# Kernel optimization log

Measured on AMD Instinct MI355X. Metric: run time of the kernel, lower is better.

Reference implementation:

```python
import jax, jax.numpy as jnp
import numpy as np
from jax import lax

# config (matches init_kwargs)
HEADS = 4
KD2 = 256          # key_dim // 2
KNN = 16
BLOCK = 128        # knn * block_rate
COL = 512          # value_size // block
VALUE_SIZE = 65536 # key_num ** 2
D_OUT = 512
D_IN = 1024
QUERYDIM = HEADS * KD2  # 1024
KERNEL = 3


def setup_inputs() -> dict:
    key = jax.random.key(0)
    ks = jax.random.split(key, 8)
    B, T = 2, 2048
    return {
        "x": jax.random.normal(ks[0], (B, T, D_IN), dtype=jnp.float32),
        "conv_w": jax.random.normal(ks[1], (D_IN, 1, KERNEL), dtype=jnp.float32) * 0.1,
        "conv_b": jax.random.normal(ks[2], (D_IN,), dtype=jnp.float32) * 0.1,
        "lin_w": jax.random.normal(ks[3], (QUERYDIM, D_IN), dtype=jnp.float32) * (D_IN ** -0.5),
        "lin_b": jax.random.normal(ks[4], (QUERYDIM,), dtype=jnp.float32) * 0.1,
        "rowkeys": jax.random.normal(ks[5], (BLOCK, HEADS, KD2), dtype=jnp.float32) * (KD2 ** -0.5),
        "colkeys": jax.random.normal(ks[6], (COL, HEADS, KD2), dtype=jnp.float32) * (KD2 ** -0.5),
        "value_w": jax.random.normal(ks[7], (VALUE_SIZE, D_OUT), dtype=jnp.float32),
    }


def _forward(x, conv_w, conv_b, lin_w, lin_b, rowkeys, colkeys, value_w):
    B, T, C = x.shape
    # --- Querynet: causal depthwise conv1d + linear ---
    xt = jnp.transpose(x, (0, 2, 1))  # (B, C, T)
    y = lax.conv_general_dilated(
        xt, conv_w, window_strides=(1,), padding=[(KERNEL - 1, 0)],
        feature_group_count=C, dimension_numbers=("NCH", "OIH", "NCH"))
    y = y + conv_b[None, :, None]
    y = jnp.transpose(y, (0, 2, 1))                     # (B, T, C)
    query = y @ lin_w.T + lin_b                         # (B, T, querydim)
    # torch: query.view(B, heads, T, key_dim//2) -- raw C-order reshape
    q = query.reshape(B, HEADS, T, KD2)
    # --- block_wise_choice.get_indices ---
    score = jnp.einsum("bhtd,ehd->bhte", q, rowkeys)    # (B,H,T,block)
    col_scores = jnp.einsum("bhtd,chd->bhtc", q, colkeys)  # (B,H,T,col)
    score_col, idx_col = lax.top_k(col_scores, 1)       # (B,H,T,1)
    base = jnp.arange(BLOCK, dtype=jnp.int32)
    indices = base[None, None, None, :] * COL + idx_col  # (B,H,T,block)
    score = score + score_col                            # broadcast add
    # torch .view(B,H,-1,T): raw C-order reshape mixing tokens and blocks
    score = score.reshape(B, HEADS, BLOCK, T)
    indices = indices.reshape(B, HEADS, BLOCK, T)
    k = T * KNN // BLOCK
    score_top, dispatch = lax.top_k(score, k)            # (B,H,block,k), sorted desc
    idx_top = jnp.take_along_axis(indices, dispatch, axis=-1)
    score_r = score_top.reshape(B, BLOCK, -1)            # (B, block, H*k)
    idx_r = idx_top.reshape(B, BLOCK, -1)
    disp_r = dispatch.reshape(B, BLOCK, -1)
    # --- Memory_value: gather-weight-scatter ---
    gathered = value_w[idx_r]                            # (B, block, H*k, d)
    weighted = (gathered * score_r[..., None]).reshape(B, -1, D_OUT)
    flat_disp = disp_r.reshape(B, -1)                    # values in [0, T)
    out = jnp.zeros((B, T, D_OUT), dtype=weighted.dtype)
    out = out.at[jnp.arange(B)[:, None], flat_disp].add(weighted)
    return out


def reference(x, conv_w, conv_b, lin_w, lin_b, rowkeys, colkeys, value_w):
    return _forward(x, conv_w, conv_b, lin_w, lin_b, rowkeys, colkeys, value_w)
```

## Files before the change

kernel.cpp:

```cpp
#include <hip/hip_runtime.h>

constexpr int Bc   = 2;
constexpr int Tc   = 2048;
constexpr int Cc   = 1024;
constexpr int QDc  = 1024;
constexpr int Hc   = 4;
constexpr int KD2c = 256;
constexpr int BLKc = 128;
constexpr int COLc = 512;
constexpr int DOUTc= 512;
constexpr int KSELc= 256;
constexpr int NKEYS= BLKc + COLc;
constexpr int NBINS= Bc * Tc;
constexpr int NSEL = Bc * Hc * BLKc * KSELc;

typedef short bf16x8 __attribute__((ext_vector_type(8)));
typedef float f32x4  __attribute__((ext_vector_type(4)));

__device__ __forceinline__ unsigned short f2bf(float f) {
    unsigned u = __float_as_uint(f);
    u += 0x7FFFu + ((u >> 16) & 1u);
    return (unsigned short)(u >> 16);
}
__device__ __forceinline__ float bf2f(unsigned short h) {
    return __uint_as_float((unsigned)h << 16);
}
__device__ __forceinline__ void splitbf3(float f, unsigned short* h,
                                         unsigned short* m, unsigned short* l) {
    unsigned short hh = f2bf(f);
    float r1 = f - bf2f(hh);
    unsigned short mm = f2bf(r1);
    float r2 = r1 - bf2f(mm);
    *h = hh; *m = mm; *l = f2bf(r2);
}

__device__ __forceinline__ void gld_lds16(const void* g, void* l) {
    __builtin_amdgcn_global_load_lds(
        (const __attribute__((address_space(1))) unsigned int*)g,
        (__attribute__((address_space(3))) unsigned int*)l, 16, 0, 0);
}

__global__ __launch_bounds__(256) void conv_kernel(
    const float* __restrict__ x, const float* __restrict__ cw,
    const float* __restrict__ cb, unsigned short* __restrict__ y1,
    unsigned short* __restrict__ y2, unsigned short* __restrict__ y3)
{
    int idx = blockIdx.x * 256 + threadIdx.x;
    int c = idx & (Cc - 1);
    int t = (idx >> 10) & (Tc - 1);
    int b = idx >> 21;
    float w0 = cw[c*3+0], w1 = cw[c*3+1], w2 = cw[c*3+2];
    const float* xb = x + (size_t)b * Tc * Cc;
    float acc = cb[c] + w2 * xb[(size_t)t*Cc + c];
    if (t >= 1) acc += w1 * xb[(size_t)(t-1)*Cc + c];
    if (t >= 2) acc += w0 * xb[(size_t)(t-2)*Cc + c];
    splitbf3(acc, &y1[idx], &y2[idx], &y3[idx]);
}

__global__ __launch_bounds__(256) void convw_kernel(
    const float* __restrict__ w, unsigned short* __restrict__ w1,
    unsigned short* __restrict__ w2, unsigned short* __restrict__ w3)
{
    int idx = blockIdx.x * 256 + threadIdx.x;
    splitbf3(w[idx], &w1[idx], &w2[idx], &w3[idx]);
}

__global__ __launch_bounds__(256) void convkeys_kernel(
    const float* __restrict__ rowkeys, const float* __restrict__ colkeys,
    unsigned short* __restrict__ k1, unsigned short* __restrict__ k2,
    unsigned short* __restrict__ k3)
{
    int bid = blockIdx.x;
    int h = bid / NKEYS, n = bid % NKEYS;
    int k = threadIdx.x;
    float v = (n < BLKc) ? rowkeys[((size_t)n*Hc + h)*KD2c + k]
                         : colkeys[((size_t)(n-BLKc)*Hc + h)*KD2c + k];
    size_t o = ((size_t)h*NKEYS + n)*KD2c + k;
    splitbf3(v, &k1[o], &k2[o], &k3[o]);
}

__device__ __forceinline__ void mfma_gemm_tile(
    const unsigned short* __restrict__ A1g, const unsigned short* __restrict__ A2g,
    const unsigned short* __restrict__ A3g, int lda,
    const unsigned short* __restrict__ B1g, const unsigned short* __restrict__ B2g,
    const unsigned short* __restrict__ B3g, int ldb,
    int K, int m0, int n0, char* lds, f32x4 acc[4][4])
{
    const int tid  = threadIdx.x;
    const int wave = tid >> 6, lane = tid & 63;
    const int wr = wave >> 1, wc = wave & 1;
    const int g = lane >> 4, r16 = lane & 15;

    int aoff[4], boff[4];
    #pragma unroll
    for (int i = 0; i < 4; i++) {
        int ra = wr*64 + i*16 + r16;
        aoff[i] = ra*64 + ((g ^ ((ra>>1)&3)) << 4);
        int rb = wc*64 + i*16 + r16;
        boff[i] = rb*64 + ((g ^ ((rb>>1)&3)) << 4);
    }
    const int c0 = wave*64 + lane;
    const int c1 = 256 + c0;
    const int row0 = c0 >> 2, kg0 = ((c0 & 3) ^ ((row0>>1)&3)) * 8;
    const int row1 = c1 >> 2, kg1 = ((c1 & 3) ^ ((row1>>1)&3)) * 8;
    char* d0 = lds + wave*1024;
    char* d1 = lds + 4096 + wave*1024;

#define STAGE(kc, bo) do {                                                 \
        size_t a0_ = (size_t)(m0+row0)*lda + (kc) + kg0;                   \
        size_t a1_ = (size_t)(m0+row1)*lda + (kc) + kg1;                   \
        size_t b0_ = (size_t)(n0+row0)*ldb + (kc) + kg0;                   \
        size_t b1_ = (size_t)(n0+row1)*ldb + (kc) + kg1;                   \
        gld_lds16(A1g + a0_, d0 + (bo));                                   \
        gld_lds16(A1g + a1_, d1 + (bo));                                   \
        gld_lds16(A2g + a0_, d0 + 8192 + (bo));                            \
        gld_lds16(A2g + a1_, d1 + 8192 + (bo));                            \
        gld_lds16(A3g + a0_, d0 + 16384 + (bo));                           \
        gld_lds16(A3g + a1_, d1 + 16384 + (bo));                           \
        gld_lds16(B1g + b0_, d0 + 24576 + (bo));                           \
        gld_lds16(B1g + b1_, d1 + 24576 + (bo));                           \
        gld_lds16(B2g + b0_, d0 + 32768 + (bo));                           \
        gld_lds16(B2g + b1_, d1 + 32768 + (bo));                           \
        gld_lds16(B3g + b0_, d0 + 40960 + (bo));                           \
        gld_lds16(B3g + b1_, d1 + 40960 + (bo));                           \
    } while (0)

    auto compute = [&](int bo) {
        bf16x8 a1[4], a2[4], a3[4], b1[4], b2[4], b3[4];
        #pragma unroll
        for (int i = 0; i < 4; i++) {
            a1[i] = *(const bf16x8*)(lds + bo + aoff[i]);
            a2[i] = *(const bf16x8*)(lds + bo +  8192 + aoff[i]);
            a3[i] = *(const bf16x8*)(lds + bo + 16384 + aoff[i]);
            b1[i] = *(const bf16x8*)(lds + bo + 24576 + boff[i]);
            b2[i] = *(const bf16x8*)(lds + bo + 32768 + boff[i]);
            b3[i] = *(const bf16x8*)(lds + bo + 40960 + boff[i]);
        }
        #pragma unroll
        for (int i = 0; i < 4; i++)
            #pragma unroll
            for (int j = 0; j < 4; j++) {
                acc[i][j] = __builtin_amdgcn_mfma_f32_16x16x32_bf16(a3[i], b1[j], acc[i][j], 0, 0, 0);
                acc[i][j] = __builtin_amdgcn_mfma_f32_16x16x32_bf16(a2[i], b2[j], acc[i][j], 0, 0, 0);
                acc[i][j] = __builtin_amdgcn_mfma_f32_16x16x32_bf16(a1[i], b3[j], acc[i][j], 0, 0, 0);
                acc[i][j] = __builtin_amdgcn_mfma_f32_16x16x32_bf16(a2[i], b1[j], acc[i][j], 0, 0, 0);
                acc[i][j] = __builtin_amdgcn_mfma_f32_16x16x32_bf16(a1[i], b2[j], acc[i][j], 0, 0, 0);
                acc[i][j] = __builtin_amdgcn_mfma_f32_16x16x32_bf16(a1[i], b1[j], acc[i][j], 0, 0, 0);
            }
    };

    const int NT = K / 32;
    STAGE(0, 0);
    int bo = 0;
    for (int t = 0; t < NT - 1; ++t) {
        STAGE((t+1)*32, bo ^ 49152);
        asm volatile("s_waitcnt vmcnt(12)" ::: "memory");
        __builtin_amdgcn_s_barrier();
        asm volatile("" ::: "memory");
        compute(bo);
        asm volatile("" ::: "memory");
        __builtin_amdgcn_s_barrier();
        bo ^= 49152;
    }
    asm volatile("s_waitcnt vmcnt(0)" ::: "memory");
    __builtin_amdgcn_s_barrier();
    asm volatile("" ::: "memory");
    compute(bo);
#undef STAGE
}

__global__ __launch_bounds__(256) void qgemm_kernel(
    const unsigned short* __restrict__ y1, const unsigned short* __restrict__ y2,
    const unsigned short* __restrict__ y3,
    const unsigned short* __restrict__ w1, const unsigned short* __restrict__ w2,
    const unsigned short* __restrict__ w3,
    const float* __restrict__ bias,
    unsigned short* __restrict__ q1, unsigned short* __restrict__ q2,
    unsigned short* __restrict__ q3)
{
    __shared__ char lds[98304];
    int m0 = blockIdx.y * 128, n0 = blockIdx.x * 128;
    f32x4 acc[4][4];
    #pragma unroll
    for (int i = 0; i < 4; i++)
        #pragma unroll
        for (int j = 0; j < 4; j++) acc[i][j] = (f32x4)0.f;
    mfma_gemm_tile(y1, y2, y3, Cc, w1, w2, w3, Cc, Cc, m0, n0, lds, acc);

    const int lane = threadIdx.x & 63, wave = threadIdx.x >> 6;
    const int wr = wave >> 1, wc = wave & 1;
    const int g = lane >> 4, r16 = lane & 15;
    #pragma unroll
    for (int i = 0; i < 4; i++)
        #pragma unroll
        for (int j = 0; j < 4; j++)
            #pragma unroll
            for (int reg = 0; reg < 4; reg++) {
                int m = m0 + wr*64 + i*16 + g*4 + reg;
                int n = n0 + wc*64 + j*16 + r16;
                float v = acc[i][j][reg] + bias[n];
                size_t o = (size_t)m * QDc + n;
                splitbf3(v, &q1[o], &q2[o], &q3[o]);
            }
}

__global__ __launch_bounds__(256) void sgemm_kernel(
    const unsigned short* __restrict__ q1, const unsigned short* __restrict__ q2,
    const unsigned short* __restrict__ q3,
    const unsigned short* __restrict__ k1, const unsigned short* __restrict__ k2,
    const unsigned short* __restrict__ k3,
    float* __restrict__ Ctmp)
{
    __shared__ char lds[98304];
    int b4h = blockIdx.z;
    size_t qo = (size_t)b4h * (Tc * KD2c);
    size_t ko = (size_t)(b4h & 3) * (NKEYS * KD2c);
    int m0 = blockIdx.y * 128, n0 = blockIdx.x * 128;
    f32x4 acc[4][4];
    #pragma unroll
    for (int i = 0; i < 4; i++)
        #pragma unroll
        for (int j = 0; j < 4; j++) acc[i][j] = (f32x4)0.f;
    mfma_gemm_tile(q1+qo, q2+qo, q3+qo, KD2c, k1+ko, k2+ko, k3+ko, KD2c,
                   KD2c, m0, n0, lds, acc);

    const int lane = threadIdx.x & 63, wave = threadIdx.x >> 6;
    const int wr = wave >> 1, wc = wave & 1;
    const int g = lane >> 4, r16 = lane & 15;
    float* Cb = Ctmp + (size_t)b4h * Tc * NKEYS;
    #pragma unroll
    for (int i = 0; i < 4; i++)
        #pragma unroll
        for (int j = 0; j < 4; j++)
            #pragma unroll
            for (int reg = 0; reg < 4; reg++) {
                int m = m0 + wr*64 + i*16 + g*4 + reg;
                int n = n0 + wc*64 + j*16 + r16;
                Cb[(size_t)m * NKEYS + n] = acc[i][j][reg];
            }
}

__global__ __launch_bounds__(256) void colmax_kernel(
    const float* __restrict__ Ctmp, float* __restrict__ s, int* __restrict__ cidx)
{
    int rid = blockIdx.x * 4 + (threadIdx.x >> 6);
    int lane = threadIdx.x & 63;
    const float* row = Ctmp + (size_t)rid * NKEYS;
    float best = -3.4e38f; int bi = 0;
    #pragma unroll
    for (int i = 0; i < 8; i++) {
        int c = lane + i*64;
        float v = row[BLKc + c];
        if (v > best) { best = v; bi = c; }
    }
    #pragma unroll
    for (int off = 32; off > 0; off >>= 1) {
        float ov = __shfl_xor(best, off, 64);
        int   oi = __shfl_xor(bi,   off, 64);
        if (ov > best || (ov == best && oi < bi)) { best = ov; bi = oi; }
    }
    if (lane == 0) cidx[rid] = bi;
    #pragma unroll
    for (int e = lane; e < BLKc; e += 64)
        s[(size_t)rid*BLKc + e] = row[e] + best;
}

__global__ __launch_bounds__(256) void topk_kernel(
    const float* __restrict__ s, const int* __restrict__ cidx,
    int* __restrict__ tk_j, int* __restrict__ tk_vidx, float* __restrict__ tk_score)
{
    int wid  = (blockIdx.x << 2) + (threadIdx.x >> 6);
    int lane = threadIdx.x & 63;
    int batch = wid >> 7;
    int i = wid & 127;
    const float* srow = s + (size_t)batch * (Tc*BLKc) + (size_t)i * 2048;

    unsigned key[8][4];
    #pragma unroll
    for (int r = 0; r < 8; r++) {
        float4 v4 = *(const float4*)&srow[r*256 + lane*4];
        float vv[4] = {v4.x, v4.y, v4.z, v4.w};
        #pragma unroll
        for (int e = 0; e < 4; e++) {
            unsigned u = __float_as_uint(vv[e]);
            key[r][e] = (u >> 31) ? ~u : (u | 0x80000000u);
        }
    }

    unsigned lo = 0, hi = 0xFFFFFFFFu;
    while (lo < hi) {
        unsigned d = hi - lo;
        unsigned mid = lo + ((d >> 1) + (d & 1u));
        int cnt = 0;
        #pragma unroll
        for (int r = 0; r < 8; r++)
            #pragma unroll
            for (int e = 0; e < 4; e++)
                cnt += (key[r][e] >= mid) ? 1 : 0;
        #pragma unroll
        for (int off = 32; off > 0; off >>= 1) cnt += __shfl_xor(cnt, off, 64);
        if (cnt >= KSELc) lo = mid; else hi = mid - 1;
    }
    const unsigned thr = lo;

    int gcnt = 0, ecnt = 0;
    unsigned eqmask = 0;
    #pragma unroll
    for (int r = 0; r < 8; r++)
        #pragma unroll
        for (int e = 0; e < 4; e++) {
            gcnt += (key[r][e] > thr) ? 1 : 0;
            if (key[r][e] == thr) { eqmask |= (1u << (r*4+e)); ecnt++; }
        }

    int gpre = gcnt, epre = ecnt;
    #pragma unroll
    for (int off = 1; off < 64; off <<= 1) {
        int gv = __shfl_up(gpre, off, 64);
        int ev = __shfl_up(epre, off, 64);
        if (lane >= off) { gpre += gv; epre += ev; }
    }
    const int total_greater = __shfl(gpre, 63, 64);
    const int total_eq      = __shfl(epre, 63, 64);
    const int gbase = gpre - gcnt;
    const int ebase = epre - ecnt;
    const int need  = KSELc - total_greater;

    const size_t obase = (size_t)wid * KSELc;
    const int cbase = batch * Tc + i * 16;

    int rk = 0;
    #pragma unroll
    for (int r = 0; r < 8; r++)
        #pragma unroll
        for (int e = 0; e < 4; e++) {
            if (key[r][e] > thr) {
                int j = r*256 + lane*4 + e;
                unsigned u = key[r][e];
                float f = (u >> 31) ? __uint_as_float(u ^ 0x80000000u)
                                    : __uint_as_float(~u);
                size_t o = obase + gbase + rk;
                tk_j[o] = j;
                tk_vidx[o] = (j & 127) * COLc + cidx[cbase + (j >> 7)];
                tk_score[o] = f;
                rk++;
            }
        }

    if (need == total_eq) {
        int erk = 0;
        #pragma unroll
        for (int r = 0; r < 8; r++)
            #pragma unroll
            for (int e = 0; e < 4; e++) {
                if (key[r][e] == thr) {
                    int j = r*256 + lane*4 + e;
                    float f = (thr >> 31) ? __uint_as_float(thr ^ 0x80000000u)
                                          : __uint_as_float(~thr);
                    size_t o = obase + total_greater + ebase + erk;
                    tk_j[o] = j;
                    tk_vidx[o] = (j & 127) * COLc + cidx[cbase + (j >> 7)];
                    tk_score[o] = f;
                    erk++;
                }
            }
    } else {
        unsigned em = eqmask;
        int left = need;
        while (left > 0) {
            int myj = 0x7FFFFFFF;
            if (em) {
                int bit = __builtin_ctz(em);
                myj = (bit >> 2)*256 + lane*4 + (bit & 3);
            }
            int mn = myj;
            #pragma unroll
            for (int off = 32; off > 0; off >>= 1) mn = min(mn, __shfl_xor(mn, off, 64));
            if (myj == mn) {
                em &= em - 1;
                int j = mn;
                float f = (thr >> 31) ? __uint_as_float(thr ^ 0x80000000u)
                                      : __uint_as_float(~thr);
                size_t o = obase + (KSELc - left);
                tk_j[o] = j;
                tk_vidx[o] = (j & 127) * COLc + cidx[cbase + (j >> 7)];
                tk_score[o] = f;
            }
            left--;
        }
    }
}

__global__ __launch_bounds__(256) void zero_bins_kernel(int* __restrict__ p, int n)
{
    int i = blockIdx.x * 256 + threadIdx.x;
    if (i < n) p[i] = 0;
}

__global__ __launch_bounds__(256) void count_kernel(
    const int* __restrict__ tk_j, int* __restrict__ counts)
{
    int idx = blockIdx.x * 256 + threadIdx.x;
    int r = idx >> 8;
    int b = r >> 9;
    int j = tk_j[idx];
    atomicAdd(&counts[b * Tc + j], 1);
}

__global__ __launch_bounds__(256) void scan_kernel(
    const int* __restrict__ counts, int* __restrict__ offsets)
{
    __shared__ int part[256];
    int tid = threadIdx.x;
    int local[16];
    int sum = 0;
    #pragma unroll
    for (int k = 0; k < 16; k++) { local[k] = sum; sum += counts[tid*16 + k]; }
    part[tid] = sum;
    __syncthreads();
    for (int st = 1; st < 256; st <<= 1) {
        int v = (tid >= st) ? part[tid - st] : 0;
        __syncthreads();
        part[tid] += v;
        __syncthreads();
    }
    int base = (tid == 0) ? 0 : part[tid - 1];
    #pragma unroll
    for (int k = 0; k < 16; k++) offsets[tid*16 + k] = base + local[k];
    if (tid == 255) offsets[NBINS] = base + sum;
}

__global__ __launch_bounds__(256) void fill_kernel(
    const int* __restrict__ tk_j, const int* __restrict__ tk_vidx,
    const float* __restrict__ tk_score, const int* __restrict__ offsets,
    int* __restrict__ fillctr, int* __restrict__ bin_vidx,
    float* __restrict__ bin_score)
{
    int idx = blockIdx.x * 256 + threadIdx.x;
    int r = idx >> 8;
    int b = r >> 9;
    int bin = b * Tc + tk_j[idx];
    int pos = offsets[bin] + atomicAdd(&fillctr[bin], 1);
    bin_vidx[pos]  = tk_vidx[idx];
    bin_score[pos] = tk_score[idx];
}

__global__ __launch_bounds__(256) void gather_kernel(
    const int* __restrict__ offsets, const int* __restrict__ bin_vidx,
    const float* __restrict__ bin_score, const float* __restrict__ value_w,
    float* __restrict__ out)
{
    __shared__ int   svidx[512];
    __shared__ float sscore[512];
    int bin = blockIdx.x;
    int tid = threadIdx.x;
    int beg = offsets[bin], cnt = offsets[bin + 1] - beg;
    for (int n = tid; n < cnt; n += 256) {
        svidx[n]  = bin_vidx[beg + n];
        sscore[n] = bin_score[beg + n];
    }
    __syncthreads();

    const int c = tid * 2;
    float accx = 0.f, accy = 0.f;
    int n = 0;
    for (; n + 4 <= cnt; n += 4) {
        int   v0 = svidx[n],    v1 = svidx[n+1],  v2 = svidx[n+2],  v3 = svidx[n+3];
        float s0 = sscore[n],   s1 = sscore[n+1], s2 = sscore[n+2], s3 = sscore[n+3];
        float2 a = *(const float2*)&value_w[(size_t)v0 * DOUTc + c];
        float2 b = *(const float2*)&value_w[(size_t)v1 * DOUTc + c];
        float2 d = *(const float2*)&value_w[(size_t)v2 * DOUTc + c];
        float2 e = *(const float2*)&value_w[(size_t)v3 * DOUTc + c];
        accx += s0*a.x; accy += s0*a.y;
        accx += s1*b.x; accy += s1*b.y;
        accx += s2*d.x; accy += s2*d.y;
        accx += s3*e.x; accy += s3*e.y;
    }
    for (; n < cnt; n++) {
        int v = svidx[n]; float sc = sscore[n];
        float2 a = *(const float2*)&value_w[(size_t)v * DOUTc + c];
        accx += sc*a.x; accy += sc*a.y;
    }
    float2 res; res.x = accx; res.y = accy;
    *(float2*)&out[(size_t)bin * DOUTc + c] = res;
}

extern "C" void kernel_launch(void* const* d_in, const int* in_sizes, int n_in,
                              void* d_out, int out_size, void* d_ws, size_t ws_size,
                              hipStream_t stream)
{
    const float* x       = (const float*)d_in[0];
    const float* conv_w  = (const float*)d_in[1];
    const float* conv_b  = (const float*)d_in[2];
    const float* lin_w   = (const float*)d_in[3];
    const float* lin_b   = (const float*)d_in[4];
    const float* rowkeys = (const float*)d_in[5];
    const float* colkeys = (const float*)d_in[6];
    const float* value_w = (const float*)d_in[7];
    float* out = (float*)d_out;

    constexpr size_t MB = 1024*1024;
    char* w = (char*)d_ws;
    float*          Ctmp = (float*)(w);
    unsigned short* y1   = (unsigned short*)(w);
    unsigned short* y2   = (unsigned short*)(w +  8*MB);
    unsigned short* y3   = (unsigned short*)(w + 16*MB);
    unsigned short* w1   = (unsigned short*)(w + 24*MB);
    unsigned short* w2   = (unsigned short*)(w + 26*MB);
    unsigned short* w3   = (unsigned short*)(w + 28*MB);
    unsigned short* q1   = (unsigned short*)(w + 40*MB);
    unsigned short* q2   = (unsigned short*)(w + 48*MB);
    unsigned short* q3   = (unsigned short*)(w + 56*MB);
    unsigned short* k1   = (unsigned short*)(w + 64*MB);
    unsigned short* k2   = (unsigned short*)(w + 66*MB);
    unsigned short* k3   = (unsigned short*)(w + 68*MB);
    float*          s    = (float*)(w + 70*MB);
    int*            cidx = (int*)  (w + 78*MB);
    int*            tk_j = (int*)  (w + 79*MB);
    int*            tk_v = (int*)  (w + 80*MB);
    float*          tk_s = (float*)(w + 81*MB);
    int*            counts    = (int*)  (w + 82*MB);
    int*            offsets   = (int*)  (w + 82*MB + 32768);
    int*            fillctr   = (int*)  (w + 82*MB + 65536);
    int*            bin_vidx  = (int*)  (w + 82*MB + 131072);
    float*          bin_score = (float*)(w + 82*MB + 131072 + 1048576);

    conv_kernel<<<(Bc*Tc*Cc)/256, 256, 0, stream>>>(x, conv_w, conv_b, y1, y2, y3);
    convw_kernel<<<(QDc*Cc)/256, 256, 0, stream>>>(lin_w, w1, w2, w3);
    convkeys_kernel<<<Hc*NKEYS, 256, 0, stream>>>(rowkeys, colkeys, k1, k2, k3);
    qgemm_kernel<<<dim3(QDc/128, (Bc*Tc)/128), 256, 0, stream>>>(
        y1, y2, y3, w1, w2, w3, lin_b, q1, q2, q3);
    sgemm_kernel<<<dim3(NKEYS/128, Tc/128, Bc*Hc), 256, 0, stream>>>(
        q1, q2, q3, k1, k2, k3, Ctmp);
    colmax_kernel<<<(Bc*Hc*Tc)/4, 256, 0, stream>>>(Ctmp, s, cidx);
    topk_kernel<<<Bc*Hc*BLKc/4, 256, 0, stream>>>(s, cidx, tk_j, tk_v, tk_s);
    zero_bins_kernel<<<(96*1024/4 + 255)/256, 256, 0, stream>>>(counts, 96*1024/4);
    count_kernel<<<NSEL/256, 256, 0, stream>>>(tk_j, counts);
    scan_kernel<<<1, 256, 0, stream>>>(counts, offsets);
    fill_kernel<<<NSEL/256, 256, 0, stream>>>(tk_j, tk_v, tk_s, offsets,
                                              fillctr, bin_vidx, bin_score);
    gather_kernel<<<NBINS, 256, 0, stream>>>(offsets, bin_vidx, bin_score,
                                             value_w, out);
}
```

Before: 255.1 us.

## Use 8 waves per GEMM tile and deepen gather loop unrolling

```diff
diff --git a/kernel.cpp b/kernel.cpp
--- a/kernel.cpp
+++ b/kernel.cpp
@@ -84,62 +84,56 @@
     const unsigned short* __restrict__ A3g, int lda,
     const unsigned short* __restrict__ B1g, const unsigned short* __restrict__ B2g,
     const unsigned short* __restrict__ B3g, int ldb,
-    int K, int m0, int n0, char* lds, f32x4 acc[4][4])
+    int K, int m0, int n0, char* lds, f32x4 acc[4][2])
 {
     const int tid  = threadIdx.x;
     const int wave = tid >> 6, lane = tid & 63;
-    const int wr = wave >> 1, wc = wave & 1;
+    const int wr = wave >> 2, wc = wave & 3;
     const int g = lane >> 4, r16 = lane & 15;
 
-    int aoff[4], boff[4];
+    int aoff[4], boff[2];
     #pragma unroll
     for (int i = 0; i < 4; i++) {
         int ra = wr*64 + i*16 + r16;
         aoff[i] = ra*64 + ((g ^ ((ra>>1)&3)) << 4);
-        int rb = wc*64 + i*16 + r16;
-        boff[i] = rb*64 + ((g ^ ((rb>>1)&3)) << 4);
-    }
-    const int c0 = wave*64 + lane;
-    const int c1 = 256 + c0;
-    const int row0 = c0 >> 2, kg0 = ((c0 & 3) ^ ((row0>>1)&3)) * 8;
-    const int row1 = c1 >> 2, kg1 = ((c1 & 3) ^ ((row1>>1)&3)) * 8;
+    }
+    #pragma unroll
+    for (int j = 0; j < 2; j++) {
+        int rb = wc*32 + j*16 + r16;
+        boff[j] = rb*64 + ((g ^ ((rb>>1)&3)) << 4);
+    }
+    const int row0 = tid >> 2, kg0 = ((tid & 3) ^ ((row0>>1)&3)) * 8;
     char* d0 = lds + wave*1024;
-    char* d1 = lds + 4096 + wave*1024;
 
 #define STAGE(kc, bo) do {                                                 \
         size_t a0_ = (size_t)(m0+row0)*lda + (kc) + kg0;                   \
-        size_t a1_ = (size_t)(m0+row1)*lda + (kc) + kg1;                   \
         size_t b0_ = (size_t)(n0+row0)*ldb + (kc) + kg0;                   \
-        size_t b1_ = (size_t)(n0+row1)*ldb + (kc) + kg1;                   \
         gld_lds16(A1g + a0_, d0 + (bo));                                   \
-        gld_lds16(A1g + a1_, d1 + (bo));                                   \
         gld_lds16(A2g + a0_, d0 + 8192 + (bo));                            \
-        gld_lds16(A2g + a1_, d1 + 8192 + (bo));                            \
         gld_lds16(A3g + a0_, d0 + 16384 + (bo));                           \
-        gld_lds16(A3g + a1_, d1 + 16384 + (bo));                           \
         gld_lds16(B1g + b0_, d0 + 24576 + (bo));                           \
-        gld_lds16(B1g + b1_, d1 + 24576 + (bo));                           \
         gld_lds16(B2g + b0_, d0 + 32768 + (bo));                           \
-        gld_lds16(B2g + b1_, d1 + 32768 + (bo));                           \
         gld_lds16(B3g + b0_, d0 + 40960 + (bo));                           \
-        gld_lds16(B3g + b1_, d1 + 40960 + (bo));                           \
     } while (0)
 
     auto compute = [&](int bo) {
-        bf16x8 a1[4], a2[4], a3[4], b1[4], b2[4], b3[4];
+        bf16x8 a1[4], a2[4], a3[4], b1[2], b2[2], b3[2];
         #pragma unroll
         for (int i = 0; i < 4; i++) {
             a1[i] = *(const bf16x8*)(lds + bo + aoff[i]);
             a2[i] = *(const bf16x8*)(lds + bo +  8192 + aoff[i]);
             a3[i] = *(const bf16x8*)(lds + bo + 16384 + aoff[i]);
-            b1[i] = *(const bf16x8*)(lds + bo + 24576 + boff[i]);
-            b2[i] = *(const bf16x8*)(lds + bo + 32768 + boff[i]);
-            b3[i] = *(const bf16x8*)(lds + bo + 40960 + boff[i]);
+        }
+        #pragma unroll
+        for (int j = 0; j < 2; j++) {
+            b1[j] = *(const bf16x8*)(lds + bo + 24576 + boff[j]);
+            b2[j] = *(const bf16x8*)(lds + bo + 32768 + boff[j]);
+            b3[j] = *(const bf16x8*)(lds + bo + 40960 + boff[j]);
         }
         #pragma unroll
         for (int i = 0; i < 4; i++)
             #pragma unroll
-            for (int j = 0; j < 4; j++) {
+            for (int j = 0; j < 2; j++) {
                 acc[i][j] = __builtin_amdgcn_mfma_f32_16x16x32_bf16(a3[i], b1[j], acc[i][j], 0, 0, 0);
                 acc[i][j] = __builtin_amdgcn_mfma_f32_16x16x32_bf16(a2[i], b2[j], acc[i][j], 0, 0, 0);
                 acc[i][j] = __builtin_amdgcn_mfma_f32_16x16x32_bf16(a1[i], b3[j], acc[i][j], 0, 0, 0);
@@ -154,7 +148,7 @@
     int bo = 0;
     for (int t = 0; t < NT - 1; ++t) {
         STAGE((t+1)*32, bo ^ 49152);
-        asm volatile("s_waitcnt vmcnt(12)" ::: "memory");
+        asm volatile("s_waitcnt vmcnt(6)" ::: "memory");
         __builtin_amdgcn_s_barrier();
         asm volatile("" ::: "memory");
         compute(bo);
@@ -169,7 +163,7 @@
 #undef STAGE
 }
 
-__global__ __launch_bounds__(256) void qgemm_kernel(
+__global__ __launch_bounds__(512) void qgemm_kernel(
     const unsigned short* __restrict__ y1, const unsigned short* __restrict__ y2,
     const unsigned short* __restrict__ y3,
     const unsigned short* __restrict__ w1, const unsigned short* __restrict__ w2,
@@ -180,31 +174,31 @@
 {
     __shared__ char lds[98304];
     int m0 = blockIdx.y * 128, n0 = blockIdx.x * 128;
-    f32x4 acc[4][4];
+    f32x4 acc[4][2];
     #pragma unroll
     for (int i = 0; i < 4; i++)
         #pragma unroll
-        for (int j = 0; j < 4; j++) acc[i][j] = (f32x4)0.f;
+        for (int j = 0; j < 2; j++) acc[i][j] = (f32x4)0.f;
     mfma_gemm_tile(y1, y2, y3, Cc, w1, w2, w3, Cc, Cc, m0, n0, lds, acc);
 
     const int lane = threadIdx.x & 63, wave = threadIdx.x >> 6;
-    const int wr = wave >> 1, wc = wave & 1;
+    const int wr = wave >> 2, wc = wave & 3;
     const int g = lane >> 4, r16 = lane & 15;
     #pragma unroll
     for (int i = 0; i < 4; i++)
         #pragma unroll
-        for (int j = 0; j < 4; j++)
+        for (int j = 0; j < 2; j++)
             #pragma unroll
             for (int reg = 0; reg < 4; reg++) {
                 int m = m0 + wr*64 + i*16 + g*4 + reg;
-                int n = n0 + wc*64 + j*16 + r16;
+                int n = n0 + wc*32 + j*16 + r16;
                 float v = acc[i][j][reg] + bias[n];
                 size_t o = (size_t)m * QDc + n;
                 splitbf3(v, &q1[o], &q2[o], &q3[o]);
             }
 }
 
-__global__ __launch_bounds__(256) void sgemm_kernel(
+__global__ __launch_bounds__(512) void sgemm_kernel(
     const unsigned short* __restrict__ q1, const unsigned short* __restrict__ q2,
     const unsigned short* __restrict__ q3,
     const unsigned short* __restrict__ k1, const unsigned short* __restrict__ k2,
@@ -216,26 +210,26 @@
     size_t qo = (size_t)b4h * (Tc * KD2c);
     size_t ko = (size_t)(b4h & 3) * (NKEYS * KD2c);
     int m0 = blockIdx.y * 128, n0 = blockIdx.x * 128;
-    f32x4 acc[4][4];
+    f32x4 acc[4][2];
     #pragma unroll
     for (int i = 0; i < 4; i++)
         #pragma unroll
-        for (int j = 0; j < 4; j++) acc[i][j] = (f32x4)0.f;
+        for (int j = 0; j < 2; j++) acc[i][j] = (f32x4)0.f;
     mfma_gemm_tile(q1+qo, q2+qo, q3+qo, KD2c, k1+ko, k2+ko, k3+ko, KD2c,
                    KD2c, m0, n0, lds, acc);
 
     const int lane = threadIdx.x & 63, wave = threadIdx.x >> 6;
-    const int wr = wave >> 1, wc = wave & 1;
+    const int wr = wave >> 2, wc = wave & 3;
     const int g = lane >> 4, r16 = lane & 15;
     float* Cb = Ctmp + (size_t)b4h * Tc * NKEYS;
     #pragma unroll
     for (int i = 0; i < 4; i++)
         #pragma unroll
-        for (int j = 0; j < 4; j++)
+        for (int j = 0; j < 2; j++)
             #pragma unroll
             for (int reg = 0; reg < 4; reg++) {
                 int m = m0 + wr*64 + i*16 + g*4 + reg;
-                int n = n0 + wc*64 + j*16 + r16;
+                int n = n0 + wc*32 + j*16 + r16;
                 Cb[(size_t)m * NKEYS + n] = acc[i][j][reg];
             }
 }
@@ -464,17 +458,15 @@
     const int c = tid * 2;
     float accx = 0.f, accy = 0.f;
     int n = 0;
-    for (; n + 4 <= cnt; n += 4) {
-        int   v0 = svidx[n],    v1 = svidx[n+1],  v2 = svidx[n+2],  v3 = svidx[n+3];
-        float s0 = sscore[n],   s1 = sscore[n+1], s2 = sscore[n+2], s3 = sscore[n+3];
-        float2 a = *(const float2*)&value_w[(size_t)v0 * DOUTc + c];
-        float2 b = *(const float2*)&value_w[(size_t)v1 * DOUTc + c];
-        float2 d = *(const float2*)&value_w[(size_t)v2 * DOUTc + c];
-        float2 e = *(const float2*)&value_w[(size_t)v3 * DOUTc + c];
-        accx += s0*a.x; accy += s0*a.y;
-        accx += s1*b.x; accy += s1*b.y;
-        accx += s2*d.x; accy += s2*d.y;
-        accx += s3*e.x; accy += s3*e.y;
+    for (; n + 8 <= cnt; n += 8) {
+        int vi[8]; float sc[8]; float2 vv[8];
+        #pragma unroll
+        for (int k = 0; k < 8; k++) { vi[k] = svidx[n+k]; sc[k] = sscore[n+k]; }
+        #pragma unroll
+        for (int k = 0; k < 8; k++)
+            vv[k] = *(const float2*)&value_w[(size_t)vi[k] * DOUTc + c];
+        #pragma unroll
+        for (int k = 0; k < 8; k++) { accx += sc[k]*vv[k].x; accy += sc[k]*vv[k].y; }
     }
     for (; n < cnt; n++) {
         int v = svidx[n]; float sc = sscore[n];
@@ -528,9 +520,9 @@
     conv_kernel<<<(Bc*Tc*Cc)/256, 256, 0, stream>>>(x, conv_w, conv_b, y1, y2, y3);
     convw_kernel<<<(QDc*Cc)/256, 256, 0, stream>>>(lin_w, w1, w2, w3);
     convkeys_kernel<<<Hc*NKEYS, 256, 0, stream>>>(rowkeys, colkeys, k1, k2, k3);
-    qgemm_kernel<<<dim3(QDc/128, (Bc*Tc)/128), 256, 0, stream>>>(
+    qgemm_kernel<<<dim3(QDc/128, (Bc*Tc)/128), 512, 0, stream>>>(
         y1, y2, y3, w1, w2, w3, lin_b, q1, q2, q3);
-    sgemm_kernel<<<dim3(NKEYS/128, Tc/128, Bc*Hc), 256, 0, stream>>>(
+    sgemm_kernel<<<dim3(NKEYS/128, Tc/128, Bc*Hc), 512, 0, stream>>>(
         q1, q2, q3, k1, k2, k3, Ctmp);
     colmax_kernel<<<(Bc*Hc*Tc)/4, 256, 0, stream>>>(Ctmp, s, cidx);
     topk_kernel<<<Bc*Hc*BLKc/4, 256, 0, stream>>>(s, cidx, tk_j, tk_v, tk_s);
```

New measurement: 237.3 us. 7.0% less time.
